# Optimization experiments

Measured on AMD Instinct MI355X. Metric: run time of the kernel, lower is better.

The kernel has to match this reference:

```python
import jax, jax.numpy as jnp
import numpy as np

IN_FEATURES = 4096
OUT_FEATURES = 11008

def setup_inputs() -> dict:
    key = jax.random.key(0)
    k_in, k_w, k_s, k_b = jax.random.split(key, 4)
    inp = jax.random.normal(k_in, (4, 2048, IN_FEATURES), dtype=jnp.float32)
    # int8 quantized weight [out, in]
    weight = jax.random.randint(k_w, (OUT_FEATURES, IN_FEATURES), -127, 128, dtype=jnp.int8)
    # per-output-row scales [out, 1]
    scales = jax.random.uniform(k_s, (OUT_FEATURES, 1), dtype=jnp.float32) * 0.02 + 0.001
    bias = jax.random.normal(k_b, (OUT_FEATURES,), dtype=jnp.float32) * 0.01
    return {"input": inp, "weight": weight, "scales": scales, "bias": bias}

def reference(input, weight, scales, bias):
    # Dequantize: int8 -> core dtype, then per-row scale.  [out, in]
    dequantized_weight = weight.astype(input.dtype) * scales
    # F.linear: input @ W^T + b
    out = jnp.einsum('bsi,oi->bso', input, dequantized_weight) + bias
    return out
```

## Files before the change

kernel.cpp:

```cpp
#include <hip/hip_runtime.h>
#include <stdint.h>

#define M_TOT 8192
#define K_TOT 4096
#define N_TOT 11008
#define BM 256
#define BN 256
#define BK 128
#define NT2 (K_TOT / BK)

typedef __attribute__((ext_vector_type(4))) float f32x4;
typedef __attribute__((ext_vector_type(4))) int i32x4;

__global__ __launch_bounds__(256) void quant_a(const float* __restrict__ a,
                                               int8_t* __restrict__ o,
                                               float* __restrict__ sa) {
  const int row = blockIdx.x;
  const int tid = threadIdx.x;
  const float* ap = a + (size_t)row * K_TOT + tid * 16;
  float4 v[4];
#pragma unroll
  for (int i = 0; i < 4; ++i) v[i] = *(const float4*)(ap + i * 4);
  float m = 0.f;
#pragma unroll
  for (int i = 0; i < 4; ++i) {
    m = fmaxf(m, fmaxf(fmaxf(fabsf(v[i].x), fabsf(v[i].y)),
                       fmaxf(fabsf(v[i].z), fabsf(v[i].w))));
  }
#pragma unroll
  for (int off = 32; off >= 1; off >>= 1)
    m = fmaxf(m, __shfl_xor(m, off));
  __shared__ float red[4];
  if ((tid & 63) == 0) red[tid >> 6] = m;
  __syncthreads();
  float am = fmaxf(fmaxf(red[0], red[1]), fmaxf(red[2], red[3]));
  float inv = am > 0.f ? 127.0f / am : 0.f;
  if (tid == 0) sa[row] = am > 0.f ? am / 127.0f : 0.f;
  union { int8_t b[16]; int4 q; } r;
#pragma unroll
  for (int i = 0; i < 4; ++i) {
    float4 w = v[i];
    r.b[i * 4 + 0] = (int8_t)(int)rintf(w.x * inv);
    r.b[i * 4 + 1] = (int8_t)(int)rintf(w.y * inv);
    r.b[i * 4 + 2] = (int8_t)(int)rintf(w.z * inv);
    r.b[i * 4 + 3] = (int8_t)(int)rintf(w.w * inv);
  }
  *(int4*)(o + (size_t)row * K_TOT + tid * 16) = r.q;
}

__global__ __launch_bounds__(256) void pack_w(const int* __restrict__ w,
                                              int8_t* __restrict__ o, int n16) {
  int stride = gridDim.x * 256;
  for (int i = blockIdx.x * 256 + threadIdx.x; i < n16; i += stride) {
    const int4* p = (const int4*)(w + (size_t)i * 16);
    int4 v0 = p[0], v1 = p[1], v2 = p[2], v3 = p[3];
    int4 r;
    r.x = (v0.x & 0xff) | ((v0.y & 0xff) << 8) | ((v0.z & 0xff) << 16) | (v0.w << 24);
    r.y = (v1.x & 0xff) | ((v1.y & 0xff) << 8) | ((v1.z & 0xff) << 16) | (v1.w << 24);
    r.z = (v2.x & 0xff) | ((v2.y & 0xff) << 8) | ((v2.z & 0xff) << 16) | (v2.w << 24);
    r.w = (v3.x & 0xff) | ((v3.y & 0xff) << 8) | ((v3.z & 0xff) << 16) | (v3.w << 24);
    *(int4*)(o + (size_t)i * 16) = r;
  }
}

#define VM6 asm volatile("s_waitcnt vmcnt(6)" ::: "memory");
#define VM4 asm volatile("s_waitcnt vmcnt(4)" ::: "memory");
#define VM2 asm volatile("s_waitcnt vmcnt(2)" ::: "memory");
#define VM0 asm volatile("s_waitcnt vmcnt(0)" ::: "memory");
#define BAR __builtin_amdgcn_s_barrier();

#define BODY(QM, QN, ...) do {                                                    \
  if ((QN) == 0) {                                                                \
    _Pragma("unroll") for (int mf = 0; mf < 4; ++mf) {                            \
      afr[mf][0] = *(const i32x4*)(la + (QM) * 8192 + mf * 2048 + aoff0);         \
      afr[mf][1] = *(const i32x4*)(la + (QM) * 8192 + mf * 2048 + aoff1);         \
    }                                                                             \
  }                                                                               \
  _Pragma("unroll") for (int nf = 0; nf < 2; ++nf) {                              \
    bfr[nf][0] = *(const i32x4*)(lb + (QN) * 4096 + nf * 2048 + boff0);           \
    bfr[nf][1] = *(const i32x4*)(lb + (QN) * 4096 + nf * 2048 + boff1);           \
  }                                                                               \
  __VA_ARGS__                                                                     \
  __builtin_amdgcn_s_setprio(1);                                                  \
  _Pragma("unroll") for (int mf = 0; mf < 4; ++mf)                                \
    _Pragma("unroll") for (int nf = 0; nf < 2; ++nf) {                            \
      acc[(QM)*4+mf][(QN)*2+nf] = __builtin_amdgcn_mfma_i32_16x16x64_i8(          \
          afr[mf][0], bfr[nf][0], acc[(QM)*4+mf][(QN)*2+nf], 0, 0, 0);            \
      acc[(QM)*4+mf][(QN)*2+nf] = __builtin_amdgcn_mfma_i32_16x16x64_i8(          \
          afr[mf][1], bfr[nf][1], acc[(QM)*4+mf][(QN)*2+nf], 0, 0, 0);            \
    }                                                                             \
  __builtin_amdgcn_s_setprio(0);                                                  \
} while (0)

__global__ __launch_bounds__(512, 2) void gemm_i8(
    const int8_t* __restrict__ A,
    const int8_t* __restrict__ W,
    const float* __restrict__ sa,
    const float* __restrict__ scales,
    const float* __restrict__ bias,
    float* __restrict__ out) {
  __shared__ __attribute__((aligned(16))) char lds[2][2][32768];

  const int tid = threadIdx.x;
  const int lane = tid & 63;
  const int wid = tid >> 6;
  const int wm = wid >> 2;
  const int wn = wid & 3;
  const int l15 = lane & 15;
  const int l4 = lane >> 4;
  const int xm = l15 & 7;

  const int bid = blockIdx.x;
  const int swz = (bid & 7) * 172 + (bid >> 3);
  const int g = swz / 172;
  const int rem = swz - g * 172;
  const int mq = rem / 43;
  const int mt = g * 4 + mq;
  const int nt = rem - mq * 43;

  const int r = tid >> 3;
  const int csrc = (tid & 7) ^ (r & 7);
  const int8_t* a_src = A + ((size_t)(mt * 256 + r)) * K_TOT + csrc * 16;
  const int8_t* b_src = W + ((size_t)(nt * 256 + r)) * K_TOT + csrc * 16;
  const int d_off = r * 128 + (tid & 7) * 16;

  const int pc0 = l4 ^ xm;
  const int pc1 = pc0 ^ 4;
  const int aoff0 = (wm * 128 + l15) * 128 + pc0 * 16;
  const int aoff1 = (wm * 128 + l15) * 128 + pc1 * 16;
  const int boff0 = (wn * 64 + l15) * 128 + pc0 * 16;
  const int boff1 = (wn * 64 + l15) * 128 + pc1 * 16;

  auto STG = [&](int o, int q, int t) {
    const int8_t* s = (o ? b_src : a_src) + (size_t)q * 64 * K_TOT + t * BK;
    char* d = &lds[t & 1][o][q * 8192 + d_off];
    __builtin_amdgcn_global_load_lds(
        (const __attribute__((address_space(1))) void*)s,
        (__attribute__((address_space(3))) void*)d, 16, 0, 0);
  };

  i32x4 acc[8][4];
#pragma unroll
  for (int i = 0; i < 8; ++i)
#pragma unroll
    for (int j = 0; j < 4; ++j) {
      i32x4 z = {0, 0, 0, 0};
      acc[i][j] = z;
    }
  i32x4 afr[4][2], bfr[2][2];

  STG(0, 0, 0); STG(0, 2, 0);
  STG(1, 0, 0); STG(1, 1, 0);
  STG(1, 2, 0); STG(1, 3, 0);
  STG(0, 1, 0); STG(0, 3, 0);
  STG(0, 0, 1); STG(0, 2, 1);

  for (int w = 0; w < NT2 - 2; ++w) {
    const char* la = &lds[w & 1][0][0];
    const char* lb = &lds[w & 1][1][0];
    VM4 BAR
    BODY(0, 0, STG(1, 0, w + 1); STG(1, 1, w + 1););
    BODY(0, 1, STG(1, 2, w + 1); STG(1, 3, w + 1););
    VM6 BAR
    BODY(1, 0, STG(0, 1, w + 1); STG(0, 3, w + 1););
    BODY(1, 1, STG(0, 0, w + 2); STG(0, 2, w + 2););
  }
  {
    const int w = NT2 - 2;
    const char* la = &lds[w & 1][0][0];
    const char* lb = &lds[w & 1][1][0];
    VM4 BAR
    BODY(0, 0, STG(1, 0, NT2 - 1); STG(1, 1, NT2 - 1););
    BODY(0, 1, STG(1, 2, NT2 - 1); STG(1, 3, NT2 - 1););
    VM6 BAR
    BODY(1, 0, STG(0, 1, NT2 - 1); STG(0, 3, NT2 - 1););
    BODY(1, 1, );
  }
  {
    const int w = NT2 - 1;
    const char* la = &lds[w & 1][0][0];
    const char* lb = &lds[w & 1][1][0];
    VM2 BAR
    BODY(0, 0, );
    BODY(0, 1, );
    VM0 BAR
    BODY(1, 0, );
    BODY(1, 1, );
  }

#pragma unroll
  for (int nf = 0; nf < 4; ++nf) {
    int n_g = nt * 256 + wn * 64 + nf * 16 + l15;
    float s = scales[n_g];
    float b = bias[n_g];
#pragma unroll
    for (int mf = 0; mf < 8; ++mf) {
      int m0 = mt * 256 + wm * 128 + mf * 16 + l4 * 4;
      float* op = out + (size_t)m0 * N_TOT + n_g;
#pragma unroll
      for (int j = 0; j < 4; ++j)
        op[(size_t)j * N_TOT] = (float)acc[mf][nf][j] * (sa[m0 + j] * s) + b;
    }
  }
}

__global__ __launch_bounds__(256) void naive_gemm(
    const float* __restrict__ a, const int* __restrict__ w,
    const float* __restrict__ scales, const float* __restrict__ bias,
    float* __restrict__ out) {
  size_t total = (size_t)M_TOT * N_TOT;
  size_t stride = (size_t)gridDim.x * 256;
  for (size_t idx = (size_t)blockIdx.x * 256 + threadIdx.x; idx < total; idx += stride) {
    size_t m = idx / N_TOT, n = idx - m * N_TOT;
    const float* ap = a + m * K_TOT;
    const int* wp = w + n * K_TOT;
    float s = 0.f;
    for (int k = 0; k < K_TOT; ++k) s += ap[k] * (float)wp[k];
    out[idx] = s * scales[n] + bias[n];
  }
}

extern "C" void kernel_launch(void* const* d_in, const int* in_sizes, int n_in,
                              void* d_out, int out_size, void* d_ws, size_t ws_size,
                              hipStream_t stream) {
  const float* inp = (const float*)d_in[0];
  const int* w = (const int*)d_in[1];
  const float* sc = (const float*)d_in[2];
  const float* bi = (const float*)d_in[3];
  float* out = (float*)d_out;

  const size_t a_elems = (size_t)M_TOT * K_TOT;
  const size_t w_elems = (size_t)N_TOT * K_TOT;
  const size_t need = 32768 + a_elems + w_elems;

  if (ws_size >= need) {
    float* ws_sa = (float*)d_ws;
    int8_t* ws_a = (int8_t*)d_ws + 32768;
    int8_t* ws_w = ws_a + a_elems;
    quant_a<<<M_TOT, 256, 0, stream>>>(inp, ws_a, ws_sa);
    pack_w<<<2048, 256, 0, stream>>>(w, ws_w, (int)(w_elems / 16));
    gemm_i8<<<(M_TOT / BM) * (N_TOT / BN), 512, 0, stream>>>(ws_a, ws_w, ws_sa, sc, bi, out);
  } else {
    naive_gemm<<<4096, 256, 0, stream>>>(inp, w, sc, bi, out);
  }
}
```

Baseline: 482.0 us.

## Switch int8 GEMM to 32x32x32 MFMA with new LDS swizzle and pipeline

Replaces the 16x16x64 int8 MFMA tiling with 32x32x32 int8 MFMA. Each wave now holds 4x2 32x32 accumulators, and fragment loads and the LDS XOR swizzle are redone to match the new lane layout. The K loop is restructured to process two K tiles per iteration with pointer increments, and B is staged once per tile instead of split across halves. The goal is to cut LDS fragment reads per MFMA and raise math density, at the cost of a new swizzle that may bank-conflict and a different epilogue store pattern.

```diff
diff --git a/kernel.cpp b/kernel.cpp
--- a/kernel.cpp
+++ b/kernel.cpp
@@ -7,10 +7,10 @@
 #define BM 256
 #define BN 256
 #define BK 128
-#define NT2 (K_TOT / BK)
-
-typedef __attribute__((ext_vector_type(4))) float f32x4;
+#define NT2 32
+
 typedef __attribute__((ext_vector_type(4))) int i32x4;
+typedef __attribute__((ext_vector_type(16))) int i32x16;
 
 __global__ __launch_bounds__(256) void quant_a(const float* __restrict__ a,
                                                int8_t* __restrict__ o,
@@ -36,16 +36,16 @@
   float am = fmaxf(fmaxf(red[0], red[1]), fmaxf(red[2], red[3]));
   float inv = am > 0.f ? 127.0f / am : 0.f;
   if (tid == 0) sa[row] = am > 0.f ? am / 127.0f : 0.f;
-  union { int8_t b[16]; int4 q; } r;
+  union { int8_t b[16]; int4 q; } rr;
 #pragma unroll
   for (int i = 0; i < 4; ++i) {
     float4 w = v[i];
-    r.b[i * 4 + 0] = (int8_t)(int)rintf(w.x * inv);
-    r.b[i * 4 + 1] = (int8_t)(int)rintf(w.y * inv);
-    r.b[i * 4 + 2] = (int8_t)(int)rintf(w.z * inv);
-    r.b[i * 4 + 3] = (int8_t)(int)rintf(w.w * inv);
-  }
-  *(int4*)(o + (size_t)row * K_TOT + tid * 16) = r.q;
+    rr.b[i * 4 + 0] = (int8_t)(int)rintf(w.x * inv);
+    rr.b[i * 4 + 1] = (int8_t)(int)rintf(w.y * inv);
+    rr.b[i * 4 + 2] = (int8_t)(int)rintf(w.z * inv);
+    rr.b[i * 4 + 3] = (int8_t)(int)rintf(w.w * inv);
+  }
+  *(int4*)(o + (size_t)row * K_TOT + tid * 16) = rr.q;
 }
 
 __global__ __launch_bounds__(256) void pack_w(const int* __restrict__ w,
@@ -65,30 +65,35 @@
 
 #define VM6 asm volatile("s_waitcnt vmcnt(6)" ::: "memory");
 #define VM4 asm volatile("s_waitcnt vmcnt(4)" ::: "memory");
-#define VM2 asm volatile("s_waitcnt vmcnt(2)" ::: "memory");
 #define VM0 asm volatile("s_waitcnt vmcnt(0)" ::: "memory");
 #define BAR __builtin_amdgcn_s_barrier();
 
-#define BODY(QM, QN, ...) do {                                                    \
-  if ((QN) == 0) {                                                                \
-    _Pragma("unroll") for (int mf = 0; mf < 4; ++mf) {                            \
-      afr[mf][0] = *(const i32x4*)(la + (QM) * 8192 + mf * 2048 + aoff0);         \
-      afr[mf][1] = *(const i32x4*)(la + (QM) * 8192 + mf * 2048 + aoff1);         \
-    }                                                                             \
-  }                                                                               \
-  _Pragma("unroll") for (int nf = 0; nf < 2; ++nf) {                              \
-    bfr[nf][0] = *(const i32x4*)(lb + (QN) * 4096 + nf * 2048 + boff0);           \
-    bfr[nf][1] = *(const i32x4*)(lb + (QN) * 4096 + nf * 2048 + boff1);           \
+#define RD_A(BUF, QM, M2, KS) \
+  (*(const i32x4*)(lbase + ((BUF)*32768 + (QM)*8192 + (M2)*4096) + va[KS]))
+#define RD_B(BUF, NF, KS) \
+  (*(const i32x4*)(lbase + ((BUF)*32768 + (NF)*4096) + vb[KS]))
+
+#define STG(OP, Q, BUF, SRC) \
+  __builtin_amdgcn_global_load_lds( \
+      (const __attribute__((address_space(1))) void*)((SRC) + (size_t)(Q)*64*K_TOT), \
+      (__attribute__((address_space(3))) void*)(&lds[OP][BUF][(Q)*8192 + d_off]), 16, 0, 0);
+
+#define BODY(BUF, QM, ...) do {                                                   \
+  _Pragma("unroll") for (int m2 = 0; m2 < 2; ++m2)                                \
+    _Pragma("unroll") for (int ks = 0; ks < 4; ++ks)                              \
+      afr[m2][ks] = RD_A(BUF, QM, m2, ks);                                        \
+  if ((QM) == 0) {                                                                \
+    _Pragma("unroll") for (int nf = 0; nf < 2; ++nf)                              \
+      _Pragma("unroll") for (int ks = 0; ks < 4; ++ks)                            \
+        bfr[nf][ks] = RD_B(BUF, nf, ks);                                          \
   }                                                                               \
   __VA_ARGS__                                                                     \
   __builtin_amdgcn_s_setprio(1);                                                  \
-  _Pragma("unroll") for (int mf = 0; mf < 4; ++mf)                                \
-    _Pragma("unroll") for (int nf = 0; nf < 2; ++nf) {                            \
-      acc[(QM)*4+mf][(QN)*2+nf] = __builtin_amdgcn_mfma_i32_16x16x64_i8(          \
-          afr[mf][0], bfr[nf][0], acc[(QM)*4+mf][(QN)*2+nf], 0, 0, 0);            \
-      acc[(QM)*4+mf][(QN)*2+nf] = __builtin_amdgcn_mfma_i32_16x16x64_i8(          \
-          afr[mf][1], bfr[nf][1], acc[(QM)*4+mf][(QN)*2+nf], 0, 0, 0);            \
-    }                                                                             \
+  _Pragma("unroll") for (int ks = 0; ks < 4; ++ks)                                \
+    _Pragma("unroll") for (int m2 = 0; m2 < 2; ++m2)                              \
+      _Pragma("unroll") for (int nf = 0; nf < 2; ++nf)                            \
+        acc[(QM)*2 + m2][nf] = __builtin_amdgcn_mfma_i32_32x32x32_i8(             \
+            afr[m2][ks], bfr[nf][ks], acc[(QM)*2 + m2][nf], 0, 0, 0);             \
   __builtin_amdgcn_s_setprio(0);                                                  \
 } while (0)
 
@@ -106,9 +111,8 @@
   const int wid = tid >> 6;
   const int wm = wid >> 2;
   const int wn = wid & 3;
-  const int l15 = lane & 15;
-  const int l4 = lane >> 4;
-  const int xm = l15 & 7;
+  const int l31 = lane & 31;
+  const int hi = lane >> 5;
 
   const int bid = blockIdx.x;
   const int swz = (bid & 7) * 172 + (bid >> 3);
@@ -119,87 +123,75 @@
   const int nt = rem - mq * 43;
 
   const int r = tid >> 3;
-  const int csrc = (tid & 7) ^ (r & 7);
+  const int csrc = (tid & 7) ^ ((r & 3) << 1);
   const int8_t* a_src = A + ((size_t)(mt * 256 + r)) * K_TOT + csrc * 16;
   const int8_t* b_src = W + ((size_t)(nt * 256 + r)) * K_TOT + csrc * 16;
   const int d_off = r * 128 + (tid & 7) * 16;
 
-  const int pc0 = l4 ^ xm;
-  const int pc1 = pc0 ^ 4;
-  const int aoff0 = (wm * 128 + l15) * 128 + pc0 * 16;
-  const int aoff1 = (wm * 128 + l15) * 128 + pc1 * 16;
-  const int boff0 = (wn * 64 + l15) * 128 + pc0 * 16;
-  const int boff1 = (wn * 64 + l15) * 128 + pc1 * 16;
-
-  auto STG = [&](int o, int q, int t) {
-    const int8_t* s = (o ? b_src : a_src) + (size_t)q * 64 * K_TOT + t * BK;
-    char* d = &lds[t & 1][o][q * 8192 + d_off];
-    __builtin_amdgcn_global_load_lds(
-        (const __attribute__((address_space(1))) void*)s,
-        (__attribute__((address_space(3))) void*)d, 16, 0, 0);
-  };
-
-  i32x4 acc[8][4];
-#pragma unroll
-  for (int i = 0; i < 8; ++i)
-#pragma unroll
-    for (int j = 0; j < 4; ++j) {
-      i32x4 z = {0, 0, 0, 0};
-      acc[i][j] = z;
-    }
-  i32x4 afr[4][2], bfr[2][2];
-
-  STG(0, 0, 0); STG(0, 2, 0);
-  STG(1, 0, 0); STG(1, 1, 0);
-  STG(1, 2, 0); STG(1, 3, 0);
-  STG(0, 1, 0); STG(0, 3, 0);
-  STG(0, 0, 1); STG(0, 2, 1);
-
-  for (int w = 0; w < NT2 - 2; ++w) {
-    const char* la = &lds[w & 1][0][0];
-    const char* lb = &lds[w & 1][1][0];
+  int va[4], vb[4];
+#pragma unroll
+  for (int ks = 0; ks < 4; ++ks) {
+    int phys = (((ks * 2 + hi) ^ ((l31 & 3) << 1))) * 16;
+    va[ks] = (wm * 128 + l31) * 128 + phys;
+    vb[ks] = 65536 + (wn * 64 + l31) * 128 + phys;
+  }
+  const char* lbase = (const char*)&lds[0][0][0];
+
+  i32x16 acc[4][2];
+#pragma unroll
+  for (int i = 0; i < 4; ++i)
+#pragma unroll
+    for (int j = 0; j < 2; ++j)
+#pragma unroll
+      for (int e = 0; e < 16; ++e) acc[i][j][e] = 0;
+  i32x4 afr[2][4], bfr[2][4];
+
+  STG(0, 0, 0, a_src) STG(0, 2, 0, a_src)
+  STG(1, 0, 0, b_src) STG(1, 1, 0, b_src)
+  STG(1, 2, 0, b_src) STG(1, 3, 0, b_src)
+  STG(0, 1, 0, a_src) STG(0, 3, 0, a_src)
+  STG(0, 0, 1, a_src + 128) STG(0, 2, 1, a_src + 128)
+  const int8_t* a_nxt = a_src + 128;
+  const int8_t* b_nxt = b_src + 128;
+
+  for (int it = 0; it < 15; ++it) {
     VM4 BAR
-    BODY(0, 0, STG(1, 0, w + 1); STG(1, 1, w + 1););
-    BODY(0, 1, STG(1, 2, w + 1); STG(1, 3, w + 1););
+    BODY(0, 0, STG(1, 0, 1, b_nxt) STG(1, 1, 1, b_nxt)
+               STG(1, 2, 1, b_nxt) STG(1, 3, 1, b_nxt));
     VM6 BAR
-    BODY(1, 0, STG(0, 1, w + 1); STG(0, 3, w + 1););
-    BODY(1, 1, STG(0, 0, w + 2); STG(0, 2, w + 2););
-  }
-  {
-    const int w = NT2 - 2;
-    const char* la = &lds[w & 1][0][0];
-    const char* lb = &lds[w & 1][1][0];
+    BODY(0, 1, STG(0, 1, 1, a_nxt) STG(0, 3, 1, a_nxt)
+               STG(0, 0, 0, a_nxt + 128) STG(0, 2, 0, a_nxt + 128));
+    a_nxt += 128; b_nxt += 128;
     VM4 BAR
-    BODY(0, 0, STG(1, 0, NT2 - 1); STG(1, 1, NT2 - 1););
-    BODY(0, 1, STG(1, 2, NT2 - 1); STG(1, 3, NT2 - 1););
+    BODY(1, 0, STG(1, 0, 0, b_nxt) STG(1, 1, 0, b_nxt)
+               STG(1, 2, 0, b_nxt) STG(1, 3, 0, b_nxt));
     VM6 BAR
-    BODY(1, 0, STG(0, 1, NT2 - 1); STG(0, 3, NT2 - 1););
-    BODY(1, 1, );
-  }
-  {
-    const int w = NT2 - 1;
-    const char* la = &lds[w & 1][0][0];
-    const char* lb = &lds[w & 1][1][0];
-    VM2 BAR
-    BODY(0, 0, );
-    BODY(0, 1, );
-    VM0 BAR
-    BODY(1, 0, );
-    BODY(1, 1, );
-  }
-
-#pragma unroll
-  for (int nf = 0; nf < 4; ++nf) {
-    int n_g = nt * 256 + wn * 64 + nf * 16 + l15;
-    float s = scales[n_g];
-    float b = bias[n_g];
-#pragma unroll
-    for (int mf = 0; mf < 8; ++mf) {
-      int m0 = mt * 256 + wm * 128 + mf * 16 + l4 * 4;
-      float* op = out + (size_t)m0 * N_TOT + n_g;
-#pragma unroll
-      for (int j = 0; j < 4; ++j)
-        op[(size_t)j * N_TOT] = (float)acc[mf][nf][j] * (sa[m0 + j] * s) + b;
+    BODY(1, 1, STG(0, 1, 0, a_nxt) STG(0, 3, 0, a_nxt)
+               STG(0, 0, 1, a_nxt + 128) STG(0, 2, 1, a_nxt + 128));
+    a_nxt += 128; b_nxt += 128;
+  }
+  VM4 BAR
+  BODY(0, 0, STG(1, 0, 1, b_nxt) STG(1, 1, 1, b_nxt)
+             STG(1, 2, 1, b_nxt) STG(1, 3, 1, b_nxt));
+  VM6 BAR
+  BODY(0, 1, STG(0, 1, 1, a_nxt) STG(0, 3, 1, a_nxt));
+  VM0 BAR
+  BODY(1, 0, );
+  BODY(1, 1, );
+
+  const int ng0 = nt * 256 + wn * 64 + l31;
+  const float s0 = scales[ng0], s1 = scales[ng0 + 32];
+  const float b0 = bias[ng0], b1 = bias[ng0 + 32];
+#pragma unroll
+  for (int mf = 0; mf < 4; ++mf) {
+    int mb = mt * 256 + wm * 128 + mf * 32 + hi * 4;
+#pragma unroll
+    for (int reg = 0; reg < 16; ++reg) {
+      int m = mb + (reg & 3) + 8 * (reg >> 2);
+      float sm = sa[m];
+      float* row = out + (size_t)m * N_TOT;
+      row[ng0] = (float)acc[mf][0][reg] * (sm * s0) + b0;
+      row[ng0 + 32] = (float)acc[mf][1][reg] * (sm * s1) + b1;
     }
   }
 }
```

Result: slower. 542.6 us (+12.6%).
